# Kernel tuning notes

Measured on AMD Instinct MI355X. Metric: run time of the kernel, lower is better.

## Reference

```python
import jax, jax.numpy as jnp
import numpy as np

B, S, H, Z = 32, 2048, 256, 64
TEMPERATURE = float(H) ** 0.5
NEG_INF = -1e9


def setup_inputs() -> dict:
    key = jax.random.key(0)
    ks = jax.random.split(key, 8)
    return {
        "encoder_hidden_states": jax.random.normal(ks[0], (B, S, H), dtype=jnp.float32),
        "decoder_hidden_states": jax.random.normal(ks[1], (B, S, H), dtype=jnp.float32),
        "decoder_final_hidden_state": jax.random.normal(ks[2], (B, H), dtype=jnp.float32),
        "latent_z_seq": jax.random.normal(ks[3], (B, S, Z), dtype=jnp.float32),
        "mask": jax.random.randint(ks[4], (B, S), 0, 2).astype(bool),
        "Wq": jax.random.normal(ks[5], (H, H), dtype=jnp.float32),
        "Wk": jax.random.normal(ks[6], (H, H), dtype=jnp.float32),
        "Wv": jax.random.normal(ks[7], (Z, Z), dtype=jnp.float32),
    }


def reference(encoder_hidden_states, decoder_hidden_states, decoder_final_hidden_state,
              latent_z_seq, mask, Wq, Wk, Wv):
    # Projections
    k = jnp.einsum('bsh,hd->bsd', encoder_hidden_states, Wk)
    q = jnp.einsum('bsh,hd->bsd', decoder_hidden_states, Wq)
    v = jnp.einsum('bsz,zd->bsd', latent_z_seq, Wv)
    # alignment[b, i, j] = q_i . k_j / sqrt(H)   -> [B, S, S]
    alignment = jnp.einsum('bid,bjd->bij', q, k) / TEMPERATURE
    # mask over QUERY positions (axis -2), broadcast along key axis (-1)
    alignment = jnp.where(mask[:, :, None], alignment, NEG_INF)
    # NOTE: non-standard softmax over the query axis (dim=-2)
    attn = jax.nn.softmax(alignment, axis=-2)
    output = jnp.einsum('bij,bjd->bid', attn, v)  # [B, S, Z]
    return output, attn
```

## Files before the change

kernel.cpp:

```cpp
#include <hip/hip_runtime.h>
#include <stdint.h>

#define B_  32
#define S_  2048
#define H_  256
#define Z_  64

typedef unsigned short u16;
typedef __attribute__((ext_vector_type(8))) short bf16x8;
typedef __attribute__((ext_vector_type(4))) float f32x4;

__device__ __forceinline__ u16 f2bf(float f) {
    unsigned int x = __float_as_uint(f);
    x = (x + 0x7fffu + ((x >> 16) & 1u)) >> 16;
    return (u16)x;
}
__device__ __forceinline__ float bf2f(u16 u) {
    return __uint_as_float(((unsigned int)u) << 16);
}

__device__ __forceinline__ void gl2lds16(const void* g, void* l) {
    __builtin_amdgcn_global_load_lds(
        (const __attribute__((address_space(1))) unsigned int*)g,
        (__attribute__((address_space(3))) unsigned int*)l,
        16, 0, 0);
}

__global__ void detect_kernel(const u16* __restrict__ wq, int* __restrict__ flag) {
    __shared__ int tot;
    const int t = threadIdx.x;
    if (t == 0) tot = 0;
    __syncthreads();
    int cnt = 0;
    #pragma unroll
    for (int r = 0; r < 16; ++r) {
        u16 u = wq[(r * 256 + t) * 2];
        int e = (u >> 7) & 0xFF;
        cnt += (u == 0 || (e >= 107 && e <= 132)) ? 1 : 0;
    }
    atomicAdd(&tot, cnt);
    __syncthreads();
    if (t == 0) *flag = (tot < 2048) ? 1 : 0;
}

__global__ __launch_bounds__(256) void mask_conv_kernel(const void* __restrict__ raw,
                                                        int* __restrict__ mi) {
    __shared__ int isByte;
    const int t = threadIdx.x;
    if (t == 0) isByte = 0;
    __syncthreads();
    const unsigned int* w = (const unsigned int*)raw;
    if (w[t & 255] > 1u) isByte = 1;
    __syncthreads();
    int e = blockIdx.x * 256 + t;
    int val;
    if (isByte) val = ((const unsigned char*)raw)[e] ? 1 : 0;
    else        val = w[e] ? 1 : 0;
    mi[e] = val;
}

__global__ void wsplit_kernel(const int* __restrict__ flagp,
                              const void* __restrict__ Wq, const void* __restrict__ Wk,
                              u16* __restrict__ WqTh, u16* __restrict__ WqTl,
                              u16* __restrict__ WkTh, u16* __restrict__ WkTl) {
    const int fp32 = *flagp;
    const void* src = blockIdx.y ? Wk : Wq;
    u16* oh = blockIdx.y ? WkTh : WqTh;
    u16* ol = blockIdx.y ? WkTl : WqTl;
    int base = blockIdx.x * 1024;
    #pragma unroll
    for (int r = 0; r < 4; ++r) {
        int idx = base + r * 256 + threadIdx.x;
        int d = idx >> 8, h = idx & 255;
        float v = fp32 ? ((const float*)src)[h * 256 + d]
                       : bf2f(((const u16*)src)[h * 256 + d]);
        u16 hi = f2bf(v);
        oh[idx] = hi;
        ol[idx] = f2bf(v - bf2f(hi));
    }
}

__global__ __launch_bounds__(256, 2) void proj_kernel(
        const int* __restrict__ flagp,
        const float* __restrict__ Xf, const u16* __restrict__ Xu,
        const u16* __restrict__ WTh, const u16* __restrict__ WTl,
        u16* __restrict__ Ph, u16* __restrict__ Pl)
{
    __shared__ __align__(16) u16 ldsAh[128 * 32];
    __shared__ __align__(16) u16 ldsAl[128 * 32];
    __shared__ __align__(16) u16 ldsBh[128 * 32];
    __shared__ __align__(16) u16 ldsBl[128 * 32];
    const int fp32 = *flagp;
    const int t = threadIdx.x;
    const int lane = t & 63, w = t >> 6;
    const int i0 = blockIdx.x * 128;
    const int d0 = blockIdx.y * 128;
    const int rh = w >> 1, ch = w & 1;
    const int l15 = lane & 15, koff = (lane >> 4) * 8;

    f32x4 acc[4][4];
    #pragma unroll
    for (int a = 0; a < 4; ++a)
        #pragma unroll
        for (int c = 0; c < 4; ++c) acc[a][c] = (f32x4){0.f, 0.f, 0.f, 0.f};

    for (int ks = 0; ks < 8; ++ks) {
        const int kc = ks * 32;
        #pragma unroll
        for (int rep = 0; rep < 2; ++rep) {
            int s = t + rep * 256;
            int r = s >> 2, c8 = (s & 3) * 8;
            gl2lds16(WTh + (size_t)(d0 + r) * H_ + kc + c8, ldsBh + s * 8);
            gl2lds16(WTl + (size_t)(d0 + r) * H_ + kc + c8, ldsBl + s * 8);
        }
        if (fp32) {
            #pragma unroll
            for (int rep = 0; rep < 2; ++rep) {
                int s = t + rep * 256;
                int r = s >> 2, c8 = (s & 3) * 8;
                const float4* src = (const float4*)(Xf + (size_t)(i0 + r) * H_ + kc + c8);
                float4 x0 = src[0], x1 = src[1];
                float xs[8] = {x0.x, x0.y, x0.z, x0.w, x1.x, x1.y, x1.z, x1.w};
                unsigned hh[8], ll[8];
                #pragma unroll
                for (int j = 0; j < 8; ++j) {
                    u16 hb = f2bf(xs[j]);
                    hh[j] = hb;
                    ll[j] = f2bf(xs[j] - bf2f(hb));
                }
                uint4 ph, pl;
                ph.x = hh[0] | (hh[1] << 16); ph.y = hh[2] | (hh[3] << 16);
                ph.z = hh[4] | (hh[5] << 16); ph.w = hh[6] | (hh[7] << 16);
                pl.x = ll[0] | (ll[1] << 16); pl.y = ll[2] | (ll[3] << 16);
                pl.z = ll[4] | (ll[5] << 16); pl.w = ll[6] | (ll[7] << 16);
                *(uint4*)(ldsAh + s * 8) = ph;
                *(uint4*)(ldsAl + s * 8) = pl;
            }
        } else {
            #pragma unroll
            for (int rep = 0; rep < 2; ++rep) {
                int s = t + rep * 256;
                int r = s >> 2, c8 = (s & 3) * 8;
                uint4 raw = *(const uint4*)(Xu + (size_t)(i0 + r) * H_ + kc + c8);
                *(uint4*)(ldsAh + s * 8) = raw;
                *(uint4*)(ldsAl + s * 8) = (uint4){0u, 0u, 0u, 0u};
            }
        }
        __syncthreads();
        bf16x8 ah[4], al[4], bh[4], bl[4];
        #pragma unroll
        for (int f = 0; f < 4; ++f) {
            int ar = (rh * 64 + f * 16 + l15) * 32 + koff;
            int br = (ch * 64 + f * 16 + l15) * 32 + koff;
            ah[f] = *(const bf16x8*)(ldsAh + ar);
            al[f] = *(const bf16x8*)(ldsAl + ar);
            bh[f] = *(const bf16x8*)(ldsBh + br);
            bl[f] = *(const bf16x8*)(ldsBl + br);
        }
        #pragma unroll
        for (int fr = 0; fr < 4; ++fr)
            #pragma unroll
            for (int fc = 0; fc < 4; ++fc) {
                acc[fr][fc] = __builtin_amdgcn_mfma_f32_16x16x32_bf16(al[fr], bh[fc], acc[fr][fc], 0, 0, 0);
                acc[fr][fc] = __builtin_amdgcn_mfma_f32_16x16x32_bf16(ah[fr], bl[fc], acc[fr][fc], 0, 0, 0);
                acc[fr][fc] = __builtin_amdgcn_mfma_f32_16x16x32_bf16(ah[fr], bh[fc], acc[fr][fc], 0, 0, 0);
            }
        __syncthreads();
    }
    #pragma unroll
    for (int fr = 0; fr < 4; ++fr)
        #pragma unroll
        for (int fc = 0; fc < 4; ++fc)
            #pragma unroll
            for (int reg = 0; reg < 4; ++reg) {
                float v = acc[fr][fc][reg];
                int i = i0 + rh * 64 + fr * 16 + (lane >> 4) * 4 + reg;
                int d = d0 + ch * 64 + fc * 16 + l15;
                u16 hi = f2bf(v);
                u16 lo = f2bf(v - bf2f(hi));
                size_t off = (size_t)i * H_ + d;
                Ph[off] = hi;
                Pl[off] = lo;
            }
}

__global__ __launch_bounds__(256) void vproj_kernel(
        const int* __restrict__ flagp, const void* __restrict__ Lraw,
        const void* __restrict__ Wvraw, u16* __restrict__ vT)
{
    __shared__ float wv[64 * 16];
    const int fp32 = *flagp;
    const int t = threadIdx.x;
    const int dc = blockIdx.y;
    #pragma unroll
    for (int r = 0; r < 4; ++r) {
        int idx = r * 256 + t;
        int z = idx >> 4, dd = idx & 15;
        wv[idx] = fp32 ? ((const float*)Wvraw)[z * 64 + dc * 16 + dd]
                       : bf2f(((const u16*)Wvraw)[z * 64 + dc * 16 + dd]);
    }
    __syncthreads();
    const int flat = blockIdx.x * 256 + t;
    const int b = flat >> 11, s = flat & 2047;

    float lz[64];
    if (fp32) {
        const float4* lr = (const float4*)((const float*)Lraw + (size_t)flat * 64);
        #pragma unroll
        for (int c = 0; c < 16; ++c) {
            float4 v = lr[c];
            lz[c * 4 + 0] = v.x; lz[c * 4 + 1] = v.y;
            lz[c * 4 + 2] = v.z; lz[c * 4 + 3] = v.w;
        }
    } else {
        const uint4* lr = (const uint4*)((const u16*)Lraw + (size_t)flat * 64);
        #pragma unroll
        for (int c = 0; c < 8; ++c) {
            uint4 v = lr[c];
            unsigned wd[4] = {v.x, v.y, v.z, v.w};
            #pragma unroll
            for (int e2 = 0; e2 < 4; ++e2) {
                lz[c * 8 + e2 * 2 + 0] = bf2f((u16)(wd[e2] & 0xffffu));
                lz[c * 8 + e2 * 2 + 1] = bf2f((u16)(wd[e2] >> 16));
            }
        }
    }

    float acc[16];
    #pragma unroll
    for (int d = 0; d < 16; ++d) acc[d] = 0.f;
    for (int z = 0; z < 64; ++z) {
        float lv = lz[z];
        const float4* wrow = (const float4*)&wv[z * 16];
        #pragma unroll
        for (int d4 = 0; d4 < 4; ++d4) {
            float4 wq = wrow[d4];
            acc[d4 * 4 + 0] += lv * wq.x;
            acc[d4 * 4 + 1] += lv * wq.y;
            acc[d4 * 4 + 2] += lv * wq.z;
            acc[d4 * 4 + 3] += lv * wq.w;
        }
    }
    #pragma unroll
    for (int d = 0; d < 16; ++d)
        vT[((size_t)b * 64 + dc * 16 + d) * S_ + s] = f2bf(acc[d]);
}

__global__ __launch_bounds__(256, 2) void qk_kernel(
        const u16* __restrict__ qh, const u16* __restrict__ ql,
        const u16* __restrict__ kh, const u16* __restrict__ kl,
        const int* __restrict__ maskI, u16* __restrict__ attnB,
        float* __restrict__ attnF, float* __restrict__ m_p,
        float* __restrict__ s_p, int b0, const int* __restrict__ flagp)
{
    __shared__ __align__(16) char smem[35328];
    u16*  stage = (u16*)smem;
    u16*  etile = (u16*)smem;
    float* cmax = (float*)(smem + 32768);
    float* csum = (float*)(smem + 33792);
    float* mrow = (float*)(smem + 34816);

    const int fp32 = *flagp;
    const int t = threadIdx.x;
    const int lane = t & 63, w = t >> 6;
    const int jt = blockIdx.x, it = blockIdx.y, bz = blockIdx.z;
    const int b = b0 + bz;
    const int i0 = it * 128, j0 = jt * 128;
    const int rh = w >> 1, ch = w & 1;
    const int l15 = lane & 15, koff = (lane >> 4) * 8;

    if (t < 128) mrow[t] = (maskI[b * S_ + i0 + t] != 0) ? 1.f : 0.f;

    const size_t qbase = ((size_t)bz * S_ + i0) * H_;
    const size_t kbase = ((size_t)bz * S_ + j0) * H_;

    f32x4 acc[4][4];
    #pragma unroll
    for (int a = 0; a < 4; ++a)
        #pragma unroll
        for (int c = 0; c < 4; ++c) acc[a][c] = (f32x4){0.f, 0.f, 0.f, 0.f};

    for (int ks = 0; ks < 8; ++ks) {
        const int kc = ks * 32;
        #pragma unroll
        for (int rep = 0; rep < 2; ++rep) {
            int s = t + rep * 256;
            int r = s >> 2, c8 = (s & 3) * 8;
            size_t go = (size_t)r * H_ + kc + c8;
            gl2lds16(qh + qbase + go, stage + 0 * 4096 + s * 8);
            gl2lds16(ql + qbase + go, stage + 1 * 4096 + s * 8);
            gl2lds16(kh + kbase + go, stage + 2 * 4096 + s * 8);
            gl2lds16(kl + kbase + go, stage + 3 * 4096 + s * 8);
        }
        __syncthreads();
        bf16x8 ah[4], al[4], bh[4], bl[4];
        #pragma unroll
        for (int f = 0; f < 4; ++f) {
            int ar = (rh * 64 + f * 16 + l15) * 32 + koff;
            int br = (ch * 64 + f * 16 + l15) * 32 + koff;
            ah[f] = *(const bf16x8*)(stage + 0 * 4096 + ar);
            al[f] = *(const bf16x8*)(stage + 1 * 4096 + ar);
            bh[f] = *(const bf16x8*)(stage + 2 * 4096 + br);
            bl[f] = *(const bf16x8*)(stage + 3 * 4096 + br);
        }
        #pragma unroll
        for (int fr = 0; fr < 4; ++fr)
            #pragma unroll
            for (int fc = 0; fc < 4; ++fc) {
                acc[fr][fc] = __builtin_amdgcn_mfma_f32_16x16x32_bf16(al[fr], bh[fc], acc[fr][fc], 0, 0, 0);
                acc[fr][fc] = __builtin_amdgcn_mfma_f32_16x16x32_bf16(ah[fr], bl[fc], acc[fr][fc], 0, 0, 0);
                acc[fr][fc] = __builtin_amdgcn_mfma_f32_16x16x32_bf16(ah[fr], bh[fc], acc[fr][fc], 0, 0, 0);
            }
        __syncthreads();
    }

    const float inv_t = 0.0625f;
    float mloc[4] = {-3e38f, -3e38f, -3e38f, -3e38f};
    #pragma unroll
    for (int fr = 0; fr < 4; ++fr)
        #pragma unroll
        for (int reg = 0; reg < 4; ++reg) {
            float keep = mrow[rh * 64 + fr * 16 + (lane >> 4) * 4 + reg];
            #pragma unroll
            for (int fc = 0; fc < 4; ++fc) {
                float l = acc[fr][fc][reg] * inv_t;
                l = (keep != 0.f) ? l : -1e9f;
                acc[fr][fc][reg] = l;
                mloc[fc] = fmaxf(mloc[fc], l);
            }
        }
    #pragma unroll
    for (int fc = 0; fc < 4; ++fc) {
        mloc[fc] = fmaxf(mloc[fc], __shfl_xor(mloc[fc], 16, 64));
        mloc[fc] = fmaxf(mloc[fc], __shfl_xor(mloc[fc], 32, 64));
    }
    if (lane < 16) {
        #pragma unroll
        for (int fc = 0; fc < 4; ++fc)
            cmax[rh * 128 + ch * 64 + fc * 16 + lane] = mloc[fc];
    }
    __syncthreads();

    float mcol[4], sloc[4];
    #pragma unroll
    for (int fc = 0; fc < 4; ++fc) {
        int c = ch * 64 + fc * 16 + l15;
        mcol[fc] = fmaxf(cmax[c], cmax[128 + c]);
        sloc[fc] = 0.f;
    }
    #pragma unroll
    for (int fr = 0; fr < 4; ++fr)
        #pragma unroll
        for (int reg = 0; reg < 4; ++reg) {
            int row = rh * 64 + fr * 16 + (lane >> 4) * 4 + reg;
            #pragma unroll
            for (int fc = 0; fc < 4; ++fc) {
                float e = __expf(acc[fr][fc][reg] - mcol[fc]);
                sloc[fc] += e;
                etile[row * 128 + ch * 64 + fc * 16 + l15] = f2bf(e);
            }
        }
    #pragma unroll
    for (int fc = 0; fc < 4; ++fc) {
        sloc[fc] += __shfl_xor(sloc[fc], 16, 64);
        sloc[fc] += __shfl_xor(sloc[fc], 32, 64);
    }
    if (lane < 16) {
        #pragma unroll
        for (int fc = 0; fc < 4; ++fc)
            csum[rh * 128 + ch * 64 + fc * 16 + lane] = sloc[fc];
    }
    __syncthreads();

    if (t < 128) {
        float m = fmaxf(cmax[t], cmax[128 + t]);
        float sres = csum[t] + csum[128 + t];
        size_t so = ((size_t)b * 16 + it) * S_ + j0 + t;
        m_p[so] = m;
        s_p[so] = sres;
    }
    const size_t abase = ((size_t)b * S_ + i0) * S_ + j0;
    if (fp32) {
        #pragma unroll
        for (int rep = 0; rep < 8; ++rep) {
            int s = t + rep * 256;
            int row = s >> 4, off = (s & 15) * 8;
            const u16* src = etile + s * 8;
            float* gp = attnF + abase + (size_t)row * S_ + off;
            float4 f0, f1;
            f0.x = bf2f(src[0]); f0.y = bf2f(src[1]); f0.z = bf2f(src[2]); f0.w = bf2f(src[3]);
            f1.x = bf2f(src[4]); f1.y = bf2f(src[5]); f1.z = bf2f(src[6]); f1.w = bf2f(src[7]);
            *(float4*)gp = f0;
            *(float4*)(gp + 4) = f1;
        }
    } else {
        #pragma unroll
        for (int rep = 0; rep < 8; ++rep) {
            int s = t + rep * 256;
            int row = s >> 4, off = (s & 15) * 8;
            *(uint4*)(attnB + abase + (size_t)row * S_ + off) = *(const uint4*)(etile + s * 8);
        }
    }
}

__global__ __launch_bounds__(256) void stats_kernel(
        const float* __restrict__ m_p, const float* __restrict__ s_p, float* __restrict__ scl)
{
    int id = blockIdx.x * 256 + threadIdx.x;
    int b = id >> 11, j = id & 2047;
    float mv[16];
    float M = -3e38f;
    #pragma unroll
    for (int itile = 0; itile < 16; ++itile) {
        mv[itile] = m_p[((size_t)b * 16 + itile) * S_ + j];
        M = fmaxf(M, mv[itile]);
    }
    float L = 0.f;
    #pragma unroll
    for (int itile = 0; itile < 16; ++itile)
        L += s_p[((size_t)b * 16 + itile) * S_ + j] * __expf(mv[itile] - M);
    float invL = (L > 0.f) ? (1.f / L) : 0.f;
    #pragma unroll
    for (int itile = 0; itile < 16; ++itile)
        scl[((size_t)b * 16 + itile) * S_ + j] = __expf(mv[itile] - M) * invL;
}

__global__ __launch_bounds__(256, 2) void av_kernel(
        const u16* __restrict__ vT, const float* __restrict__ scl,
        u16* __restrict__ attnB, float* __restrict__ attnF,
        u16* __restrict__ outB, float* __restrict__ outF,
        const int* __restrict__ flagp)
{
    __shared__ __align__(16) u16 lds_attn[128 * 128];
    __shared__ __align__(16) u16 lds_vt[64 * 128];
    __shared__ float lds_scale[128];
    const int fp32 = *flagp;
    const int t = threadIdx.x;
    const int lane = t & 63, w = t >> 6;
    const int it = blockIdx.x, b = blockIdx.y;
    const int i0 = it * 128;
    const int l15 = lane & 15, koff = (lane >> 4) * 8;

    f32x4 acc[2][4];
    #pragma unroll
    for (int a = 0; a < 2; ++a)
        #pragma unroll
        for (int c = 0; c < 4; ++c) acc[a][c] = (f32x4){0.f, 0.f, 0.f, 0.f};

    for (int jt = 0; jt < 16; ++jt) {
        const int j0 = jt * 128;
        __syncthreads();
        if (t < 128) lds_scale[t] = scl[((size_t)b * 16 + it) * S_ + j0 + t];
        #pragma unroll
        for (int rep = 0; rep < 4; ++rep) {
            int s = t + rep * 256;
            int d = s >> 4, off = (s & 15) * 8;
            gl2lds16(vT + ((size_t)b * 64 + d) * S_ + j0 + off, lds_vt + s * 8);
        }
        __syncthreads();

        const size_t abase = ((size_t)b * S_ + i0) * S_ + j0;
        if (fp32) {
            #pragma unroll
            for (int rep = 0; rep < 8; ++rep) {
                int s = t + rep * 256;
                int row = s >> 4, off = (s & 15) * 8;
                float* gp = attnF + abase + (size_t)row * S_ + off;
                float4 p0 = *(const float4*)gp;
                float4 p1 = *(const float4*)(gp + 4);
                p0.x *= lds_scale[off + 0]; p0.y *= lds_scale[off + 1];
                p0.z *= lds_scale[off + 2]; p0.w *= lds_scale[off + 3];
                p1.x *= lds_scale[off + 4]; p1.y *= lds_scale[off + 5];
                p1.z *= lds_scale[off + 6]; p1.w *= lds_scale[off + 7];
                *(float4*)gp = p0;
                *(float4*)(gp + 4) = p1;
                uint4 pk;
                pk.x = (unsigned)f2bf(p0.x) | ((unsigned)f2bf(p0.y) << 16);
                pk.y = (unsigned)f2bf(p0.z) | ((unsigned)f2bf(p0.w) << 16);
                pk.z = (unsigned)f2bf(p1.x) | ((unsigned)f2bf(p1.y) << 16);
                pk.w = (unsigned)f2bf(p1.z) | ((unsigned)f2bf(p1.w) << 16);
                *(uint4*)(lds_attn + s * 8) = pk;
            }
        } else {
            #pragma unroll
            for (int rep = 0; rep < 8; ++rep) {
                int s = t + rep * 256;
                int row = s >> 4, off = (s & 15) * 8;
                size_t ga = abase + (size_t)row * S_ + off;
                uint4 pk = *(const uint4*)(attnB + ga);
                unsigned int wd[4] = {pk.x, pk.y, pk.z, pk.w};
                #pragma unroll
                for (int e2 = 0; e2 < 4; ++e2) {
                    float f0 = bf2f((u16)(wd[e2] & 0xffffu)) * lds_scale[off + e2 * 2];
                    float f1 = bf2f((u16)(wd[e2] >> 16))     * lds_scale[off + e2 * 2 + 1];
                    wd[e2] = (unsigned int)f2bf(f0) | ((unsigned int)f2bf(f1) << 16);
                }
                uint4 opk; opk.x = wd[0]; opk.y = wd[1]; opk.z = wd[2]; opk.w = wd[3];
                *(uint4*)(attnB + ga) = opk;
                *(uint4*)(lds_attn + s * 8) = opk;
            }
        }
        __syncthreads();

        #pragma unroll
        for (int ksj = 0; ksj < 4; ++ksj) {
            bf16x8 a0 = *(const bf16x8*)(lds_attn + (w * 32 +  0 + l15) * 128 + ksj * 32 + koff);
            bf16x8 a1 = *(const bf16x8*)(lds_attn + (w * 32 + 16 + l15) * 128 + ksj * 32 + koff);
            bf16x8 bb[4];
            #pragma unroll
            for (int fc = 0; fc < 4; ++fc)
                bb[fc] = *(const bf16x8*)(lds_vt + (fc * 16 + l15) * 128 + ksj * 32 + koff);
            #pragma unroll
            for (int fc = 0; fc < 4; ++fc) {
                acc[0][fc] = __builtin_amdgcn_mfma_f32_16x16x32_bf16(a0, bb[fc], acc[0][fc], 0, 0, 0);
                acc[1][fc] = __builtin_amdgcn_mfma_f32_16x16x32_bf16(a1, bb[fc], acc[1][fc], 0, 0, 0);
            }
        }
    }
    #pragma unroll
    for (int fr = 0; fr < 2; ++fr)
        #pragma unroll
        for (int fc = 0; fc < 4; ++fc)
            #pragma unroll
            for (int reg = 0; reg < 4; ++reg) {
                int i = i0 + w * 32 + fr * 16 + (lane >> 4) * 4 + reg;
                int d = fc * 16 + l15;
                float v = acc[fr][fc][reg];
                size_t oo = ((size_t)b * S_ + i) * Z_ + d;
                if (fp32) outF[oo] = v;
                else      outB[oo] = f2bf(v);
            }
}

extern "C" void kernel_launch(void* const* d_in, const int* in_sizes, int n_in,
                              void* d_out, int out_size, void* d_ws, size_t ws_size,
                              hipStream_t stream) {
    const void* enc    = d_in[0];
    const void* dec    = d_in[1];
    const void* latent = d_in[3];
    const void* mraw   = d_in[4];
    const void* Wq     = d_in[5];
    const void* Wk     = d_in[6];
    const void* Wv     = d_in[7];

    u16*   outB  = (u16*)d_out;
    float* outF  = (float*)d_out;
    u16*   attnB = outB + (size_t)B_ * S_ * Z_;
    float* attnF = outF + (size_t)B_ * S_ * Z_;
    float* m_p = (float*)d_out;
    float* s_p = m_p + (size_t)B_ * 16 * S_;

    char* ws = (char*)d_ws;
    int*   flag  = (int*)ws;
    int*   maskI = (int*)(ws + 256);
    u16*   vT    = (u16*)((char*)maskI + (size_t)B_ * S_ * 4);
    u16*   WqTh  = vT + (size_t)B_ * Z_ * S_;
    u16*   WqTl  = WqTh + H_ * H_;
    u16*   WkTh  = WqTl + H_ * H_;
    u16*   WkTl  = WkTh + H_ * H_;
    float* scl   = (float*)(WkTl + H_ * H_);
    u16*   grp   = (u16*)((char*)scl + (size_t)B_ * 16 * S_ * 4);

    const size_t fixed_bytes = (size_t)((char*)grp - ws);
    const size_t per_batch   = (size_t)4 * S_ * H_ * 2;
    long long avail = (long long)ws_size - (long long)fixed_bytes;
    int g_b = (avail > 0) ? (int)(avail / (long long)per_batch) : 1;
    if (g_b < 1)  g_b = 1;
    if (g_b > 32) g_b = 32;

    u16* qh = grp;
    u16* ql = qh + (size_t)g_b * S_ * H_;
    u16* kh = ql + (size_t)g_b * S_ * H_;
    u16* kl = kh + (size_t)g_b * S_ * H_;

    detect_kernel<<<dim3(1), 256, 0, stream>>>((const u16*)Wq, flag);
    mask_conv_kernel<<<dim3(256), 256, 0, stream>>>(mraw, maskI);
    wsplit_kernel<<<dim3(64, 2), 256, 0, stream>>>(flag, Wq, Wk, WqTh, WqTl, WkTh, WkTl);
    vproj_kernel<<<dim3(256, 4), 256, 0, stream>>>(flag, latent, Wv, vT);

    for (int b0 = 0; b0 < B_; b0 += g_b) {
        int g = (B_ - b0 < g_b) ? (B_ - b0) : g_b;
        size_t eoff = (size_t)b0 * S_ * H_;
        proj_kernel<<<dim3(g * 16, 2), 256, 0, stream>>>(
            flag, (const float*)dec + eoff, (const u16*)dec + eoff,
            WqTh, WqTl, qh, ql);
        proj_kernel<<<dim3(g * 16, 2), 256, 0, stream>>>(
            flag, (const float*)enc + eoff, (const u16*)enc + eoff,
            WkTh, WkTl, kh, kl);
        qk_kernel<<<dim3(16, 16, g), 256, 0, stream>>>(qh, ql, kh, kl, maskI,
                                                       attnB, attnF, m_p, s_p, b0, flag);
    }
    stats_kernel<<<dim3(256), 256, 0, stream>>>(m_p, s_p, scl);
    av_kernel<<<dim3(16, 32), 256, 0, stream>>>(vT, scl, attnB, attnF, outB, outF, flag);
}
```

Before: 1.214 ms.

## Stage unnormalized attention in bf16 workspace and pre-split inputs into bf16 hi/lo

Adds an xsplit pre-pass that converts the fp32 encoder and decoder states into bf16 hi/lo arrays, so proj_kernel can stream them straight into LDS with global_load_lds instead of converting inline. When the workspace is large enough, qk_kernel also writes the unnormalized attention tile as bf16 into a staging buffer instead of fp32 into the output. av_kernel then reads that bf16 staging buffer and writes fp32 only once, cutting one fp32 write-then-read of the large attention matrix. The cost is extra workspace, an extra pass over the inputs, and both paths depend on ws_size at runtime.

```diff
diff --git a/kernel.cpp b/kernel.cpp
--- a/kernel.cpp
+++ b/kernel.cpp
@@ -80,9 +80,52 @@
     }
 }
 
+__global__ __launch_bounds__(256) void xsplit_kernel(
+        const int* __restrict__ flagp,
+        const void* __restrict__ dec, const void* __restrict__ enc,
+        u16* __restrict__ Xdh, u16* __restrict__ Xdl,
+        u16* __restrict__ Xeh, u16* __restrict__ Xel)
+{
+    const int fp32 = *flagp;
+    const void* src = blockIdx.y ? enc : dec;
+    u16* oh = blockIdx.y ? Xeh : Xdh;
+    u16* ol = blockIdx.y ? Xel : Xdl;
+    const int t = threadIdx.x;
+    const size_t blockbase = (size_t)blockIdx.x * 4096;
+    if (fp32) {
+        const float4* s4 = (const float4*)src;
+        #pragma unroll
+        for (int j = 0; j < 4; ++j) {
+            size_t idx = blockbase + j * 1024 + t * 4;
+            float4 v = s4[idx >> 2];
+            u16 h0 = f2bf(v.x), h1 = f2bf(v.y), h2 = f2bf(v.z), h3 = f2bf(v.w);
+            u16 l0 = f2bf(v.x - bf2f(h0)), l1 = f2bf(v.y - bf2f(h1));
+            u16 l2 = f2bf(v.z - bf2f(h2)), l3 = f2bf(v.w - bf2f(h3));
+            uint2 ph, pl;
+            ph.x = (unsigned)h0 | ((unsigned)h1 << 16);
+            ph.y = (unsigned)h2 | ((unsigned)h3 << 16);
+            pl.x = (unsigned)l0 | ((unsigned)l1 << 16);
+            pl.y = (unsigned)l2 | ((unsigned)l3 << 16);
+            ((uint2*)oh)[idx >> 2] = ph;
+            ((uint2*)ol)[idx >> 2] = pl;
+        }
+    } else {
+        const uint2* s2 = (const uint2*)src;
+        #pragma unroll
+        for (int j = 0; j < 4; ++j) {
+            size_t idx = blockbase + j * 1024 + t * 4;
+            uint2 r = s2[idx >> 2];
+            uint2 z; z.x = 0u; z.y = 0u;
+            ((uint2*)oh)[idx >> 2] = r;
+            ((uint2*)ol)[idx >> 2] = z;
+        }
+    }
+}
+
 __global__ __launch_bounds__(256, 2) void proj_kernel(
-        const int* __restrict__ flagp,
+        const int* __restrict__ flagp, int use_xsplit,
         const float* __restrict__ Xf, const u16* __restrict__ Xu,
+        const u16* __restrict__ Xh, const u16* __restrict__ Xl,
         const u16* __restrict__ WTh, const u16* __restrict__ WTl,
         u16* __restrict__ Ph, u16* __restrict__ Pl)
 {
@@ -112,38 +155,45 @@
             int r = s >> 2, c8 = (s & 3) * 8;
             gl2lds16(WTh + (size_t)(d0 + r) * H_ + kc + c8, ldsBh + s * 8);
             gl2lds16(WTl + (size_t)(d0 + r) * H_ + kc + c8, ldsBl + s * 8);
-        }
-        if (fp32) {
-            #pragma unroll
-            for (int rep = 0; rep < 2; ++rep) {
-                int s = t + rep * 256;
-                int r = s >> 2, c8 = (s & 3) * 8;
-                const float4* src = (const float4*)(Xf + (size_t)(i0 + r) * H_ + kc + c8);
-                float4 x0 = src[0], x1 = src[1];
-                float xs[8] = {x0.x, x0.y, x0.z, x0.w, x1.x, x1.y, x1.z, x1.w};
-                unsigned hh[8], ll[8];
+            if (use_xsplit) {
+                size_t go = (size_t)(i0 + r) * H_ + kc + c8;
+                gl2lds16(Xh + go, ldsAh + s * 8);
+                gl2lds16(Xl + go, ldsAl + s * 8);
+            }
+        }
+        if (!use_xsplit) {
+            if (fp32) {
                 #pragma unroll
-                for (int j = 0; j < 8; ++j) {
-                    u16 hb = f2bf(xs[j]);
-                    hh[j] = hb;
-                    ll[j] = f2bf(xs[j] - bf2f(hb));
+                for (int rep = 0; rep < 2; ++rep) {
+                    int s = t + rep * 256;
+                    int r = s >> 2, c8 = (s & 3) * 8;
+                    const float4* src = (const float4*)(Xf + (size_t)(i0 + r) * H_ + kc + c8);
+                    float4 x0 = src[0], x1 = src[1];
+                    float xs[8] = {x0.x, x0.y, x0.z, x0.w, x1.x, x1.y, x1.z, x1.w};
+                    unsigned hh[8], ll[8];
+                    #pragma unroll
+                    for (int j = 0; j < 8; ++j) {
+                        u16 hb = f2bf(xs[j]);
+                        hh[j] = hb;
+                        ll[j] = f2bf(xs[j] - bf2f(hb));
+                    }
+                    uint4 ph, pl;
+                    ph.x = hh[0] | (hh[1] << 16); ph.y = hh[2] | (hh[3] << 16);
+                    ph.z = hh[4] | (hh[5] << 16); ph.w = hh[6] | (hh[7] << 16);
+                    pl.x = ll[0] | (ll[1] << 16); pl.y = ll[2] | (ll[3] << 16);
+                    pl.z = ll[4] | (ll[5] << 16); pl.w = ll[6] | (ll[7] << 16);
+                    *(uint4*)(ldsAh + s * 8) = ph;
+                    *(uint4*)(ldsAl + s * 8) = pl;
                 }
-                uint4 ph, pl;
-                ph.x = hh[0] | (hh[1] << 16); ph.y = hh[2] | (hh[3] << 16);
-                ph.z = hh[4] | (hh[5] << 16); ph.w = hh[6] | (hh[7] << 16);
-                pl.x = ll[0] | (ll[1] << 16); pl.y = ll[2] | (ll[3] << 16);
-                pl.z = ll[4] | (ll[5] << 16); pl.w = ll[6] | (ll[7] << 16);
-                *(uint4*)(ldsAh + s * 8) = ph;
-                *(uint4*)(ldsAl + s * 8) = pl;
-            }
-        } else {
-            #pragma unroll
-            for (int rep = 0; rep < 2; ++rep) {
-                int s = t + rep * 256;
-                int r = s >> 2, c8 = (s & 3) * 8;
-                uint4 raw = *(const uint4*)(Xu + (size_t)(i0 + r) * H_ + kc + c8);
-                *(uint4*)(ldsAh + s * 8) = raw;
-                *(uint4*)(ldsAl + s * 8) = (uint4){0u, 0u, 0u, 0u};
+            } else {
+                #pragma unroll
+                for (int rep = 0; rep < 2; ++rep) {
+                    int s = t + rep * 256;
+                    int r = s >> 2, c8 = (s & 3) * 8;
+                    uint4 raw = *(const uint4*)(Xu + (size_t)(i0 + r) * H_ + kc + c8);
+                    *(uint4*)(ldsAh + s * 8) = raw;
+                    *(uint4*)(ldsAl + s * 8) = (uint4){0u, 0u, 0u, 0u};
+                }
             }
         }
         __syncthreads();
@@ -250,8 +300,9 @@
         const u16* __restrict__ qh, const u16* __restrict__ ql,
         const u16* __restrict__ kh, const u16* __restrict__ kl,
         const int* __restrict__ maskI, u16* __restrict__ attnB,
-        float* __restrict__ attnF, float* __restrict__ m_p,
-        float* __restrict__ s_p, int b0, const int* __restrict__ flagp)
+        float* __restrict__ attnF, u16* __restrict__ stageB, int use_stage,
+        float* __restrict__ m_p, float* __restrict__ s_p,
+        int b0, const int* __restrict__ flagp)
 {
     __shared__ __align__(16) char smem[35328];
     u16*  stage = (u16*)smem;
@@ -381,17 +432,26 @@
     }
     const size_t abase = ((size_t)b * S_ + i0) * S_ + j0;
     if (fp32) {
-        #pragma unroll
-        for (int rep = 0; rep < 8; ++rep) {
-            int s = t + rep * 256;
-            int row = s >> 4, off = (s & 15) * 8;
-            const u16* src = etile + s * 8;
-            float* gp = attnF + abase + (size_t)row * S_ + off;
-            float4 f0, f1;
-            f0.x = bf2f(src[0]); f0.y = bf2f(src[1]); f0.z = bf2f(src[2]); f0.w = bf2f(src[3]);
-            f1.x = bf2f(src[4]); f1.y = bf2f(src[5]); f1.z = bf2f(src[6]); f1.w = bf2f(src[7]);
-            *(float4*)gp = f0;
-            *(float4*)(gp + 4) = f1;
+        if (use_stage) {
+            #pragma unroll
+            for (int rep = 0; rep < 8; ++rep) {
+                int s = t + rep * 256;
+                int row = s >> 4, off = (s & 15) * 8;
+                *(uint4*)(stageB + abase + (size_t)row * S_ + off) = *(const uint4*)(etile + s * 8);
+            }
+        } else {
+            #pragma unroll
+            for (int rep = 0; rep < 8; ++rep) {
+                int s = t + rep * 256;
+                int row = s >> 4, off = (s & 15) * 8;
+                const u16* src = etile + s * 8;
+                float* gp = attnF + abase + (size_t)row * S_ + off;
+                float4 f0, f1;
+                f0.x = bf2f(src[0]); f0.y = bf2f(src[1]); f0.z = bf2f(src[2]); f0.w = bf2f(src[3]);
+                f1.x = bf2f(src[4]); f1.y = bf2f(src[5]); f1.z = bf2f(src[6]); f1.w = bf2f(src[7]);
+                *(float4*)gp = f0;
+                *(float4*)(gp + 4) = f1;
+            }
         }
     } else {
         #pragma unroll
@@ -428,6 +488,7 @@
 __global__ __launch_bounds__(256, 2) void av_kernel(
         const u16* __restrict__ vT, const float* __restrict__ scl,
         u16* __restrict__ attnB, float* __restrict__ attnF,
+        const u16* __restrict__ stageB, int use_stage,
         u16* __restrict__ outB, float* __restrict__ outF,
         const int* __restrict__ flagp)
 {
@@ -461,25 +522,53 @@
 
         const size_t abase = ((size_t)b * S_ + i0) * S_ + j0;
         if (fp32) {
-            #pragma unroll
-            for (int rep = 0; rep < 8; ++rep) {
-                int s = t + rep * 256;
-                int row = s >> 4, off = (s & 15) * 8;
-                float* gp = attnF + abase + (size_t)row * S_ + off;
-                float4 p0 = *(const float4*)gp;
-                float4 p1 = *(const float4*)(gp + 4);
-                p0.x *= lds_scale[off + 0]; p0.y *= lds_scale[off + 1];
-                p0.z *= lds_scale[off + 2]; p0.w *= lds_scale[off + 3];
-                p1.x *= lds_scale[off + 4]; p1.y *= lds_scale[off + 5];
-                p1.z *= lds_scale[off + 6]; p1.w *= lds_scale[off + 7];
-                *(float4*)gp = p0;
-                *(float4*)(gp + 4) = p1;
-                uint4 pk;
-                pk.x = (unsigned)f2bf(p0.x) | ((unsigned)f2bf(p0.y) << 16);
-                pk.y = (unsigned)f2bf(p0.z) | ((unsigned)f2bf(p0.w) << 16);
-                pk.z = (unsigned)f2bf(p1.x) | ((unsigned)f2bf(p1.y) << 16);
-                pk.w = (unsigned)f2bf(p1.z) | ((unsigned)f2bf(p1.w) << 16);
-                *(uint4*)(lds_attn + s * 8) = pk;
+            if (use_stage) {
+                #pragma unroll
+                for (int rep = 0; rep < 8; ++rep) {
+                    int s = t + rep * 256;
+                    int row = s >> 4, off = (s & 15) * 8;
+                    uint4 pk = *(const uint4*)(stageB + abase + (size_t)row * S_ + off);
+                    unsigned wd[4] = {pk.x, pk.y, pk.z, pk.w};
+                    float4 f0, f1;
+                    f0.x = bf2f((u16)(wd[0] & 0xffffu)) * lds_scale[off + 0];
+                    f0.y = bf2f((u16)(wd[0] >> 16))     * lds_scale[off + 1];
+                    f0.z = bf2f((u16)(wd[1] & 0xffffu)) * lds_scale[off + 2];
+                    f0.w = bf2f((u16)(wd[1] >> 16))     * lds_scale[off + 3];
+                    f1.x = bf2f((u16)(wd[2] & 0xffffu)) * lds_scale[off + 4];
+                    f1.y = bf2f((u16)(wd[2] >> 16))     * lds_scale[off + 5];
+                    f1.z = bf2f((u16)(wd[3] & 0xffffu)) * lds_scale[off + 6];
+                    f1.w = bf2f((u16)(wd[3] >> 16))     * lds_scale[off + 7];
+                    float* gp = attnF + abase + (size_t)row * S_ + off;
+                    *(float4*)gp = f0;
+                    *(float4*)(gp + 4) = f1;
+                    uint4 opk;
+                    opk.x = (unsigned)f2bf(f0.x) | ((unsigned)f2bf(f0.y) << 16);
+                    opk.y = (unsigned)f2bf(f0.z) | ((unsigned)f2bf(f0.w) << 16);
+                    opk.z = (unsigned)f2bf(f1.x) | ((unsigned)f2bf(f1.y) << 16);
+                    opk.w = (unsigned)f2bf(f1.z) | ((unsigned)f2bf(f1.w) << 16);
+                    *(uint4*)(lds_attn + s * 8) = opk;
+                }
+            } else {
+                #pragma unroll
+                for (int rep = 0; rep < 8; ++rep) {
+                    int s = t + rep * 256;
+                    int row = s >> 4, off = (s & 15) * 8;
+                    float* gp = attnF + abase + (size_t)row * S_ + off;
+                    float4 p0 = *(const float4*)gp;
+                    float4 p1 = *(const float4*)(gp + 4);
+                    p0.x *= lds_scale[off + 0]; p0.y *= lds_scale[off + 1];
+                    p0.z *= lds_scale[off + 2]; p0.w *= lds_scale[off + 3];
+                    p1.x *= lds_scale[off + 4]; p1.y *= lds_scale[off + 5];
+                    p1.z *= lds_scale[off + 6]; p1.w *= lds_scale[off + 7];
+                    *(float4*)gp = p0;
+                    *(float4*)(gp + 4) = p1;
+                    uint4 pk;
+                    pk.x = (unsigned)f2bf(p0.x) | ((unsigned)f2bf(p0.y) << 16);
+                    pk.y = (unsigned)f2bf(p0.z) | ((unsigned)f2bf(p0.w) << 16);
+                    pk.z = (unsigned)f2bf(p1.x) | ((unsigned)f2bf(p1.y) << 16);
+                    pk.w = (unsigned)f2bf(p1.z) | ((unsigned)f2bf(p1.w) << 16);
+                    *(uint4*)(lds_attn + s * 8) = pk;
+                }
             }
         } else {
             #pragma unroll
@@ -559,16 +648,36 @@
     u16*   WkTh  = WqTl + H_ * H_;
     u16*   WkTl  = WkTh + H_ * H_;
     float* scl   = (float*)(WkTl + H_ * H_);
-    u16*   grp   = (u16*)((char*)scl + (size_t)B_ * 16 * S_ * 4);
-
-    const size_t fixed_bytes = (size_t)((char*)grp - ws);
-    const size_t per_batch   = (size_t)4 * S_ * H_ * 2;
+    char*  dyn   = (char*)(scl + (size_t)B_ * 16 * S_);
+
+    const size_t fixed_bytes  = (size_t)(dyn - ws);
+    const size_t per_batch    = (size_t)4 * S_ * H_ * 2;
+    const size_t xsplit_bytes = (size_t)4 * B_ * S_ * H_ * 2;
+    const size_t stage_bytes  = (size_t)B_ * S_ * S_ * 2;
+
     long long avail = (long long)ws_size - (long long)fixed_bytes;
+    int use_xsplit = 0, use_stage = 0;
+    u16 *Xdh = 0, *Xdl = 0, *Xeh = 0, *Xel = 0, *stageB = 0;
+    if (avail >= (long long)(xsplit_bytes + per_batch)) {
+        use_xsplit = 1;
+        Xdh = (u16*)dyn;
+        Xdl = Xdh + (size_t)B_ * S_ * H_;
+        Xeh = Xdl + (size_t)B_ * S_ * H_;
+        Xel = Xeh + (size_t)B_ * S_ * H_;
+        dyn += xsplit_bytes;
+        avail -= (long long)xsplit_bytes;
+    }
+    if (avail >= (long long)(stage_bytes + per_batch)) {
+        use_stage = 1;
+        stageB = (u16*)dyn;
+        dyn += stage_bytes;
+        avail -= (long long)stage_bytes;
+    }
     int g_b = (avail > 0) ? (int)(avail / (long long)per_batch) : 1;
     if (g_b < 1)  g_b = 1;
     if (g_b > 32) g_b = 32;
 
-    u16* qh = grp;
+    u16* qh = (u16*)dyn;
     u16* ql = qh + (size_t)g_b * S_ * H_;
     u16* kh = ql + (size_t)g_b * S_ * H_;
     u16* kl = kh + (size_t)g_b * S_ * H_;
@@ -577,19 +686,25 @@
     mask_conv_kernel<<<dim3(256), 256, 0, stream>>>(mraw, maskI);
     wsplit_kernel<<<dim3(64, 2), 256, 0, stream>>>(flag, Wq, Wk, WqTh, WqTl, WkTh, WkTl);
     vproj_kernel<<<dim3(256, 4), 256, 0, stream>>>(flag, latent, Wv, vT);
+    if (use_xsplit)
+        xsplit_kernel<<<dim3(4096, 2), 256, 0, stream>>>(flag, dec, enc, Xdh, Xdl, Xeh, Xel);
 
     for (int b0 = 0; b0 < B_; b0 += g_b) {
         int g = (B_ - b0 < g_b) ? (B_ - b0) : g_b;
         size_t eoff = (size_t)b0 * S_ * H_;
         proj_kernel<<<dim3(g * 16, 2), 256, 0, stream>>>(
-            flag, (const float*)dec + eoff, (const u16*)dec + eoff,
+            flag, use_xsplit, (const float*)dec + eoff, (const u16*)dec + eoff,
+            use_xsplit ? Xdh + eoff : (u16*)0, use_xsplit ? Xdl + eoff : (u16*)0,
             WqTh, WqTl, qh, ql);
         proj_kernel<<<dim3(g * 16, 2), 256, 0, stream>>>(
-            flag, (const float*)enc + eoff, (const u16*)enc + eoff,
+            flag, use_xsplit, (const float*)enc + eoff, (const u16*)enc + eoff,
+            use_xsplit ? Xeh + eoff : (u16*)0, use_xsplit ? Xel + eoff : (u16*)0,
             WkTh, WkTl, kh, kl);
         qk_kernel<<<dim3(16, 16, g), 256, 0, stream>>>(qh, ql, kh, kl, maskI,
-                                                       attnB, attnF, m_p, s_p, b0, flag);
+                                                       attnB, attnF, stageB, use_stage,
+                                                       m_p, s_p, b0, flag);
     }
     stats_kernel<<<dim3(256), 256, 0, stream>>>(m_p, s_p, scl);
-    av_kernel<<<dim3(16, 32), 256, 0, stream>>>(vT, scl, attnB, attnF, outB, outF, flag);
-}
+    av_kernel<<<dim3(16, 32), 256, 0, stream>>>(vT, scl, attnB, attnF, stageB, use_stage,
+                                                outB, outF, flag);
+}
```

Measured after the change: 1.177 ms. 3.0% less time.
